# Kernel tuning notes

Measured on AMD Instinct MI355X. Metric: run time of the kernel, lower is better.

## Reference

```python
import jax, jax.numpy as jnp
import numpy as np
import math

B, S, D_MODEL, H, CLIP = 4, 1024, 1024, 16, 16
HEAD_DIM = D_MODEL // H
NEG = -1e6


def setup_inputs() -> dict:
    key = jax.random.key(0)
    ks = jax.random.split(key, 10)
    scale = 1.0 / math.sqrt(D_MODEL)
    return {
        "queries": jax.random.normal(ks[0], (B, S, D_MODEL), jnp.float32),
        "keys": jax.random.normal(ks[1], (B, S, D_MODEL), jnp.float32),
        "values": jax.random.normal(ks[2], (B, S, D_MODEL), jnp.float32),
        "valid_lens": jax.random.randint(ks[3], (B,), 1, S + 1),
        "Wq": jax.random.normal(ks[4], (D_MODEL, D_MODEL), jnp.float32) * scale,
        "Wk": jax.random.normal(ks[5], (D_MODEL, D_MODEL), jnp.float32) * scale,
        "Wv": jax.random.normal(ks[6], (D_MODEL, D_MODEL), jnp.float32) * scale,
        "Wo": jax.random.normal(ks[7], (D_MODEL, D_MODEL), jnp.float32) * scale,
        "Ek": jax.random.normal(ks[8], (2 * CLIP + 1, HEAD_DIM), jnp.float32),
        "Ev": jax.random.normal(ks[9], (2 * CLIP + 1, HEAD_DIM), jnp.float32),
    }


def _split_heads(x):
    # [B, S, D] -> [B*H, S, head_dim]
    b, s, _ = x.shape
    return x.reshape(b, s, H, HEAD_DIM).transpose(0, 2, 1, 3).reshape(b * H, s, HEAD_DIM)


def reference(queries, keys, values, valid_lens, Wq, Wk, Wv, Wo, Ek, Ev):
    q = _split_heads(queries @ Wq.T)  # [BH, S, d]
    k = _split_heads(keys @ Wk.T)
    v = _split_heads(values @ Wv.T)

    # relative-position tables, shared across batch and heads: [Sq, Sk, d]
    rng = jnp.arange(S)
    dist = jnp.clip(rng[None, :] - rng[:, None], -CLIP, CLIP) + CLIP
    pos_k = Ek[dist]
    pos_v = Ev[dist]

    scores = jnp.einsum('bqd,bkd->bqk', q, k) + jnp.einsum('bqd,qkd->bqk', q, pos_k)
    scores = scores / math.sqrt(HEAD_DIM)

    vl = jnp.repeat(valid_lens, H)  # [B*H]
    mask = jnp.arange(S)[None, None, :] < vl[:, None, None]
    attn = jax.nn.softmax(jnp.where(mask, scores, NEG), axis=-1)

    out = jnp.einsum('bqk,bkd->bqd', attn, v) + jnp.einsum('bqk,qkd->bqd', attn, pos_v)

    # merge heads: [B*H, S, d] -> [B, S, D]
    out = out.reshape(B, H, S, HEAD_DIM).transpose(0, 2, 1, 3).reshape(B, S, D_MODEL)
    return out @ Wo.T
```

## Files before the change

### kernel.cpp

```cpp
#include <hip/hip_runtime.h>


typedef __attribute__((ext_vector_type(8))) short short8;
typedef __attribute__((ext_vector_type(4))) float floatx4;

__device__ __forceinline__ unsigned short f2bf(float f) {
  union { float f; unsigned u; } v; v.f = f;
  return (unsigned short)((v.u + 0x7fffu + ((v.u >> 16) & 1u)) >> 16);
}
__device__ __forceinline__ unsigned packbf(float lo, float hi) {
  return ((unsigned)f2bf(hi) << 16) | (unsigned)f2bf(lo);
}

__device__ __forceinline__ void gld16(const void* g, void* l) {
  __builtin_amdgcn_global_load_lds(
      (const __attribute__((address_space(1))) unsigned*)g,
      (__attribute__((address_space(3))) unsigned*)l, 16, 0, 0);
}

#define WS_XQ  ((size_t)0)
#define WS_XK  ((size_t)4194304)
#define WS_XV  ((size_t)8388608)
#define WS_W   ((size_t)12582912)
#define WS_EKB ((size_t)16777216)
#define WS_EVT ((size_t)16781312)
#define WS_QB  ((size_t)16785408)
#define WS_KB  ((size_t)20979712)
#define WS_VT  ((size_t)25174016)
#define WS_OB  ((size_t)0)

__global__ __launch_bounds__(256) void convert_all_kernel(
    const float* __restrict__ q, const float* __restrict__ k,
    const float* __restrict__ v,
    const float* __restrict__ wq, const float* __restrict__ wk,
    const float* __restrict__ wv, const float* __restrict__ wo,
    const float* __restrict__ Ek, const float* __restrict__ Ev,
    const int* __restrict__ valid_lens, unsigned short* __restrict__ ws) {
  int z = blockIdx.z;
  if (z < 3) {
    const float* src = z == 0 ? q : (z == 1 ? k : v);
    unsigned short* dst = ws + (size_t)z * 4194304;
    size_t i = ((size_t)blockIdx.x * 256 + threadIdx.x) * 8;
    if (z > 0) {
      int b = (int)(i >> 20), s = (int)((i >> 10) & 1023);
      if (s >= valid_lens[b]) return;
    }
    float4 a = *(const float4*)(src + i);
    float4 bb = *(const float4*)(src + i + 4);
    uint4 o = { packbf(a.x, a.y), packbf(a.z, a.w), packbf(bb.x, bb.y), packbf(bb.z, bb.w) };
    *(uint4*)(dst + i) = o;
  } else if (z < 7) {
    if (blockIdx.x >= 512) return;
    const float* src = (z == 3) ? wq : (z == 4 ? wk : (z == 5 ? wv : wo));
    unsigned short* dst = ws + WS_W + (size_t)(z - 3) * 1048576;
    size_t i = ((size_t)blockIdx.x * 256 + threadIdx.x) * 8;
    float4 a = *(const float4*)(src + i);
    float4 bb = *(const float4*)(src + i + 4);
    uint4 o = { packbf(a.x, a.y), packbf(a.z, a.w), packbf(bb.x, bb.y), packbf(bb.z, bb.w) };
    *(uint4*)(dst + i) = o;
  } else {
    if (blockIdx.x >= 4) return;
    int gid = blockIdx.x * 256 + threadIdx.x;
    unsigned short* ekb = ws + WS_EKB;
    int i0 = gid * 8;
    unsigned short vals[8];
#pragma unroll
    for (int u = 0; u < 8; u++) {
      int i = i0 + u;
      if (i < 4096) {
        int t = i >> 6, d = i & 63;
        vals[u] = (t < 33) ? f2bf(Ek[t * 64 + d]) : (unsigned short)0;
      } else {
        int j = i - 4096;
        int d = j >> 6, t = j & 63;
        vals[u] = (t < 33) ? f2bf(Ev[t * 64 + d]) : (unsigned short)0;
      }
    }
    *(uint4*)(ekb + i0) = *(uint4*)vals;
  }
}

__device__ __forceinline__ void gemm128_body(
    const unsigned short* __restrict__ A, const unsigned short* __restrict__ W,
    unsigned short* __restrict__ Cb, float* __restrict__ Cf, int mode, float scale) {
  __shared__ unsigned short sA[128 * 32];
  __shared__ unsigned short sB[128 * 32];
  const int tid = threadIdx.x, wave = tid >> 6, lane = tid & 63;
  const int lr = lane & 15, lq = lane >> 4;
  const int wr = wave >> 1, wc = wave & 1;
  const int m0 = blockIdx.y * 128, n0 = blockIdx.x * 128;
  const int srow = lane >> 2, scol = (lane & 3) * 8;

  const unsigned short* gA0 = A + (size_t)(m0 + wave * 16 + srow) * 1024 + scol;
  const unsigned short* gA1 = gA0 + (size_t)64 * 1024;
  const unsigned short* gB0 = W + (size_t)(n0 + wave * 16 + srow) * 1024 + scol;
  const unsigned short* gB1 = gB0 + (size_t)64 * 1024;
  unsigned short* lA0 = sA + wave * 512;  unsigned short* lA1 = lA0 + 2048;
  unsigned short* lB0 = sB + wave * 512;  unsigned short* lB1 = lB0 + 2048;

  floatx4 acc[4][4];
#pragma unroll
  for (int mi = 0; mi < 4; mi++)
#pragma unroll
    for (int ni = 0; ni < 4; ni++) acc[mi][ni] = (floatx4){0.f, 0.f, 0.f, 0.f};

  for (int k0 = 0; k0 < 1024; k0 += 32) {
    gld16(gA0 + k0, lA0); gld16(gA1 + k0, lA1);
    gld16(gB0 + k0, lB0); gld16(gB1 + k0, lB1);
    __syncthreads();
    short8 af[4], bf[4];
#pragma unroll
    for (int mi = 0; mi < 4; mi++)
      af[mi] = *(const short8*)(sA + (wr * 64 + mi * 16 + lr) * 32 + lq * 8);
#pragma unroll
    for (int ni = 0; ni < 4; ni++)
      bf[ni] = *(const short8*)(sB + (wc * 64 + ni * 16 + lr) * 32 + lq * 8);
#pragma unroll
    for (int mi = 0; mi < 4; mi++)
#pragma unroll
      for (int ni = 0; ni < 4; ni++)
        acc[mi][ni] = __builtin_amdgcn_mfma_f32_16x16x32_bf16(af[mi], bf[ni], acc[mi][ni], 0, 0, 0);
    __syncthreads();
  }

  if (mode == 2) {
#pragma unroll
    for (int mi = 0; mi < 4; mi++)
#pragma unroll
      for (int ni = 0; ni < 4; ni++) {
        int col = n0 + wc * 64 + ni * 16 + lr;
        int h = col >> 6, d = col & 63;
        int rowg = m0 + wr * 64 + mi * 16 + lq * 4;
        int b = rowg >> 10, s = rowg & 1023;
        int bh = b * 16 + h;
        uint2 pk;
        pk.x = packbf(acc[mi][ni][0], acc[mi][ni][1]);
        pk.y = packbf(acc[mi][ni][2], acc[mi][ni][3]);
        size_t off = (size_t)bh * 65536
                   + (size_t)((s >> 6) * 8 + (d >> 4) * 2 + ((s >> 5) & 1)) * 512
                   + (size_t)((((s >> 3) & 3) * 16) + (d & 15)) * 8 + (s & 7);
        *(uint2*)(Cb + off) = pk;
      }
  } else if (mode == 1) {
#pragma unroll
    for (int mi = 0; mi < 4; mi++)
#pragma unroll
      for (int ni = 0; ni < 4; ni++)
#pragma unroll
        for (int r = 0; r < 4; r++) {
          int rowg = m0 + wr * 64 + mi * 16 + lq * 4 + r;
          int col = n0 + wc * 64 + ni * 16 + lr;
          int b = rowg >> 10, s = rowg & 1023;
          int h = col >> 6, d = col & 63;
          int bh = b * 16 + h;
          size_t off = (size_t)bh * 65536
                     + (size_t)((s >> 6) * 8 + ((s & 63) >> 4) * 2 + (d >> 5)) * 512
                     + (size_t)((((d & 31) >> 3) * 16) + (s & 15)) * 8 + (d & 7);
          Cb[off] = f2bf(acc[mi][ni][r]);
        }
  } else if (mode == 3) {
#pragma unroll
    for (int mi = 0; mi < 4; mi++)
#pragma unroll
      for (int ni = 0; ni < 4; ni++)
#pragma unroll
        for (int r = 0; r < 4; r++) {
          int row = m0 + wr * 64 + mi * 16 + lq * 4 + r;
          int col = n0 + wc * 64 + ni * 16 + lr;
          Cf[(size_t)row * 1024 + col] = acc[mi][ni][r];
        }
  } else {
#pragma unroll
    for (int mi = 0; mi < 4; mi++)
#pragma unroll
      for (int ni = 0; ni < 4; ni++)
#pragma unroll
        for (int r = 0; r < 4; r++) {
          int row = m0 + wr * 64 + mi * 16 + lq * 4 + r;
          int col = n0 + wc * 64 + ni * 16 + lr;
          Cb[(size_t)row * 1024 + col] = f2bf(acc[mi][ni][r] * scale);
        }
  }
}

__global__ __launch_bounds__(256, 3) void proj_qkv_kernel(
    unsigned short* __restrict__ ws, const int* __restrict__ valid_lens) {
  int z = blockIdx.z;
  if (z > 0) {
    int m0 = blockIdx.y * 128;
    if ((m0 & 1023) >= valid_lens[m0 >> 10]) return;
  }
  const unsigned short* A = ws + (size_t)z * 4194304;
  const unsigned short* W = ws + WS_W + (size_t)z * 1048576;
  unsigned short* Cb = (z == 0) ? ws + WS_QB : (z == 1 ? ws + WS_KB : ws + WS_VT);
  int mode = (z == 2) ? 2 : (z == 0 ? 0 : 1);
  float scale = (z == 0) ? 0.125f : 1.0f;
  gemm128_body(A, W, Cb, nullptr, mode, scale);
}

__global__ __launch_bounds__(256, 3) void out_proj_kernel(
    const unsigned short* __restrict__ Ob, const unsigned short* __restrict__ Wo,
    float* __restrict__ out) {
  gemm128_body(Ob, Wo, nullptr, out, 3, 1.f);
}

__global__ __launch_bounds__(64, 2) void attn_rpr_kernel(
    const unsigned short* __restrict__ Qb, const unsigned short* __restrict__ Kf,
    const unsigned short* __restrict__ Vf, const int* __restrict__ valid_lens,
    const unsigned short* __restrict__ Ekb, const unsigned short* __restrict__ Evtb,
    unsigned short* __restrict__ Ob) {
  __shared__ unsigned short sP[32 * 72];
  __shared__ float sQE[32 * 34];
  __shared__ float sW[32 * 34];

  const int lane = threadIdx.x;
  const int lr = lane & 15, lq = lane >> 4;
  const int bh = blockIdx.x, qx = blockIdx.y;
  const int b = bh >> 4;
  const int vlen = valid_lens[b];
  const int i0 = qx * 32;
  const int colh = (bh & 15) * 64;
  const size_t bat = (size_t)b * 1024 * 1024;
  const int rbase = lq * 4;

  for (int i = lane; i < 32 * 34; i += 64) sW[i] = 0.f;

  const unsigned short* gQ = Qb + bat + (size_t)(i0 + lr) * 1024 + colh + lq * 8;
  short8 aq0[2], aq1[2];
#pragma unroll
  for (int g = 0; g < 2; g++) {
    aq0[g] = *(const short8*)(gQ + (size_t)g * 16 * 1024);
    aq1[g] = *(const short8*)(gQ + (size_t)g * 16 * 1024 + 32);
  }

#pragma unroll
  for (int ni = 0; ni < 3; ni++) {
    short8 be0 = *(const short8*)(Ekb + (ni * 16 + lr) * 64 + lq * 8);
    short8 be1 = *(const short8*)(Ekb + (ni * 16 + lr) * 64 + 32 + lq * 8);
    int t = ni * 16 + lr;
#pragma unroll
    for (int g = 0; g < 2; g++) {
      floatx4 aqe = (floatx4){0.f, 0.f, 0.f, 0.f};
      aqe = __builtin_amdgcn_mfma_f32_16x16x32_bf16(aq0[g], be0, aqe, 0, 0, 0);
      aqe = __builtin_amdgcn_mfma_f32_16x16x32_bf16(aq1[g], be1, aqe, 0, 0, 0);
      if (t < 33)
#pragma unroll
        for (int r = 0; r < 4; r++) sQE[(g * 16 + rbase + r) * 34 + t] = aqe[r];
    }
  }

  floatx4 acc_o[2][4];
#pragma unroll
  for (int g = 0; g < 2; g++)
#pragma unroll
    for (int nd = 0; nd < 4; nd++) acc_o[g][nd] = (floatx4){0.f, 0.f, 0.f, 0.f};
  float rs0[2][4] = {{0.f,0.f,0.f,0.f},{0.f,0.f,0.f,0.f}};
  float rs32[2][4] = {{0.f,0.f,0.f,0.f},{0.f,0.f,0.f,0.f}};

  const int vcl = vlen < 1024 ? vlen : 1024;
  const int kt_max = (vcl + 63) >> 6;

  const unsigned short* gKf = Kf + (size_t)bh * 65536 + lane * 8;
  const unsigned short* gVf = Vf + (size_t)bh * 65536 + lane * 8;

  for (int kt = 0; kt < kt_max; kt++) {
    const int j0 = kt * 64;

    short8 bk[4][2], bv[4][2];
#pragma unroll
    for (int ni = 0; ni < 4; ni++) {
      bk[ni][0] = *(const short8*)(gKf + (size_t)(kt * 8 + ni * 2 + 0) * 512);
      bk[ni][1] = *(const short8*)(gKf + (size_t)(kt * 8 + ni * 2 + 1) * 512);
    }
#pragma unroll
    for (int nd = 0; nd < 4; nd++) {
      bv[nd][0] = *(const short8*)(gVf + (size_t)(kt * 8 + nd * 2 + 0) * 512);
      bv[nd][1] = *(const short8*)(gVf + (size_t)(kt * 8 + nd * 2 + 1) * 512);
    }

    floatx4 accs[2][4];
    __builtin_amdgcn_s_setprio(1);
#pragma unroll
    for (int g = 0; g < 2; g++)
#pragma unroll
      for (int ni = 0; ni < 4; ni++) {
        accs[g][ni] = (floatx4){0.f, 0.f, 0.f, 0.f};
        accs[g][ni] = __builtin_amdgcn_mfma_f32_16x16x32_bf16(aq0[g], bk[ni][0], accs[g][ni], 0, 0, 0);
        accs[g][ni] = __builtin_amdgcn_mfma_f32_16x16x32_bf16(aq1[g], bk[ni][1], accs[g][ni], 0, 0, 0);
      }
    __builtin_amdgcn_s_setprio(0);

    const bool general = (j0 > i0 - 79) && (j0 < i0 + 47);
    if (!general) {
      const bool hi = (j0 >= i0 + 47);
      const int tconst = hi ? 32 : 0;
#pragma unroll
      for (int g = 0; g < 2; g++) {
        float qe[4];
#pragma unroll
        for (int r = 0; r < 4; r++) qe[r] = sQE[(g * 16 + rbase + r) * 34 + tconst];
#pragma unroll
        for (int ni = 0; ni < 4; ni++)
#pragma unroll
          for (int r = 0; r < 4; r++) {
            int j_g = j0 + ni * 16 + lr;
            float pv = (j_g < vlen) ? __expf(accs[g][ni][r] + qe[r]) : 0.f;
            if (hi) rs32[g][r] += pv; else rs0[g][r] += pv;
            sP[(g * 16 + rbase + r) * 72 + ni * 16 + lr] = f2bf(pv);
          }
      }
    } else {
#pragma unroll
      for (int g = 0; g < 2; g++)
#pragma unroll
        for (int ni = 0; ni < 4; ni++)
#pragma unroll
          for (int r = 0; r < 4; r++) {
            int i_g = i0 + g * 16 + rbase + r;
            int j_g = j0 + ni * 16 + lr;
            int dd = j_g - i_g; dd = dd < -16 ? -16 : (dd > 16 ? 16 : dd);
            int t = dd + 16;
            float pv = (j_g < vlen) ? __expf(accs[g][ni][r] + sQE[(g * 16 + rbase + r) * 34 + t]) : 0.f;
            atomicAdd(&sW[(g * 16 + rbase + r) * 34 + t], pv);
            sP[(g * 16 + rbase + r) * 72 + ni * 16 + lr] = f2bf(pv);
          }
    }

    __builtin_amdgcn_s_setprio(1);
#pragma unroll
    for (int g = 0; g < 2; g++) {
      short8 ap0 = *(const short8*)(sP + (g * 16 + lr) * 72 + lq * 8);
      short8 ap1 = *(const short8*)(sP + (g * 16 + lr) * 72 + 32 + lq * 8);
#pragma unroll
      for (int nd = 0; nd < 4; nd++) {
        acc_o[g][nd] = __builtin_amdgcn_mfma_f32_16x16x32_bf16(ap0, bv[nd][0], acc_o[g][nd], 0, 0, 0);
        acc_o[g][nd] = __builtin_amdgcn_mfma_f32_16x16x32_bf16(ap1, bv[nd][1], acc_o[g][nd], 0, 0, 0);
      }
    }
    __builtin_amdgcn_s_setprio(0);
  }

#pragma unroll
  for (int x = 1; x < 16; x <<= 1)
#pragma unroll
    for (int g = 0; g < 2; g++)
#pragma unroll
      for (int r = 0; r < 4; r++) {
        rs0[g][r] += __shfl_xor(rs0[g][r], x, 64);
        rs32[g][r] += __shfl_xor(rs32[g][r], x, 64);
      }
  if (lr == 0)
#pragma unroll
    for (int g = 0; g < 2; g++)
#pragma unroll
      for (int r = 0; r < 4; r++) {
        sW[(g * 16 + rbase + r) * 34 + 0] += rs0[g][r];
        sW[(g * 16 + rbase + r) * 34 + 32] += rs32[g][r];
      }

  {
    int row = lane >> 2;
    int c0 = (lane & 3) * 16;
    unsigned* sP32 = (unsigned*)sP;
#pragma unroll
    for (int g = 0; g < 2; g++)
#pragma unroll
      for (int q = 0; q < 8; q++) {
        int t0 = c0 + 2 * q, t1 = t0 + 1;
        float w0 = (t0 < 33) ? sW[(g * 16 + row) * 34 + t0] : 0.f;
        float w1 = (t1 < 33) ? sW[(g * 16 + row) * 34 + t1] : 0.f;
        sP32[(g * 16 + row) * 36 + (c0 >> 1) + q] = packbf(w0, w1);
      }
  }
#pragma unroll
  for (int g = 0; g < 2; g++) {
    short8 aw0 = *(const short8*)(sP + (g * 16 + lr) * 72 + lq * 8);
    short8 aw1 = *(const short8*)(sP + (g * 16 + lr) * 72 + 32 + lq * 8);
#pragma unroll
    for (int nd = 0; nd < 4; nd++) {
      short8 be0 = *(const short8*)(Evtb + (nd * 16 + lr) * 64 + lq * 8);
      short8 be1 = *(const short8*)(Evtb + (nd * 16 + lr) * 64 + 32 + lq * 8);
      acc_o[g][nd] = __builtin_amdgcn_mfma_f32_16x16x32_bf16(aw0, be0, acc_o[g][nd], 0, 0, 0);
      acc_o[g][nd] = __builtin_amdgcn_mfma_f32_16x16x32_bf16(aw1, be1, acc_o[g][nd], 0, 0, 0);
    }
  }

#pragma unroll
  for (int g = 0; g < 2; g++) {
    float linv[4];
#pragma unroll
    for (int r = 0; r < 4; r++) {
      float l = 0.f;
#pragma unroll
      for (int t = 0; t < 33; t++) l += sW[(g * 16 + rbase + r) * 34 + t];
      linv[r] = 1.f / l;
    }
#pragma unroll
    for (int nd = 0; nd < 4; nd++)
#pragma unroll
      for (int r = 0; r < 4; r++) {
        int row = i0 + g * 16 + rbase + r;
        Ob[bat + (size_t)row * 1024 + colh + nd * 16 + lr] =
            f2bf(acc_o[g][nd][r] * linv[r]);
      }
  }
}

extern "C" void kernel_launch(void* const* d_in, const int* in_sizes, int n_in,
                              void* d_out, int out_size, void* d_ws, size_t ws_size,
                              hipStream_t stream) {
  const float* queries = (const float*)d_in[0];
  const float* keys    = (const float*)d_in[1];
  const float* values  = (const float*)d_in[2];
  const int* valid_lens = (const int*)d_in[3];
  const float* Wq = (const float*)d_in[4];
  const float* Wk = (const float*)d_in[5];
  const float* Wv = (const float*)d_in[6];
  const float* Wo = (const float*)d_in[7];
  const float* Ek = (const float*)d_in[8];
  const float* Ev = (const float*)d_in[9];
  float* out = (float*)d_out;
  unsigned short* ws = (unsigned short*)d_ws;

  convert_all_kernel<<<dim3(2048, 1, 8), 256, 0, stream>>>(
      queries, keys, values, Wq, Wk, Wv, Wo, Ek, Ev, valid_lens, ws);
  proj_qkv_kernel<<<dim3(8, 32, 3), 256, 0, stream>>>(ws, valid_lens);
  attn_rpr_kernel<<<dim3(64, 32), 64, 0, stream>>>(
      ws + WS_QB, ws + WS_KB, ws + WS_VT, valid_lens, ws + WS_EKB, ws + WS_EVT, ws + WS_OB);
  out_proj_kernel<<<dim3(8, 32), 256, 0, stream>>>(ws + WS_OB, ws + WS_W + 3145728, out);
}
```

Baseline: 222.5 us.

## Use dedicated 64x128 out-proj GEMM and remap attention grid block order

Swaps the generic 128x128 GEMM body in the output projection for a dedicated 64x128-tile kernel with simple global-to-LDS loads and occupancy 4, doubling the block count to 512 to fill more CUs. The attention launch is flattened to a 1D grid, with an index remap so consecutive blocks cover all 16 heads of a batch for a given query tile, and batches are interleaved. The remap is meant to spread work across batches with different valid lengths and improve L2 locality. The new GEMM drops whatever pipelining gemm128_body had, since it syncs twice per 32-wide K step without double buffering.

Measured after the change: 212.6 us (median of 2 runs). 4.4% less time.

```diff
diff --git a/kernel.cpp b/kernel.cpp
--- a/kernel.cpp
+++ b/kernel.cpp
@@ -198,10 +198,58 @@
   gemm128_body(A, W, Cb, nullptr, mode, scale);
 }
 
-__global__ __launch_bounds__(256, 3) void out_proj_kernel(
+__global__ __launch_bounds__(256, 4) void out_proj_kernel(
     const unsigned short* __restrict__ Ob, const unsigned short* __restrict__ Wo,
     float* __restrict__ out) {
-  gemm128_body(Ob, Wo, nullptr, out, 3, 1.f);
+  __shared__ unsigned short sA[64 * 32];
+  __shared__ unsigned short sB[128 * 32];
+  const int tid = threadIdx.x, wave = tid >> 6, lane = tid & 63;
+  const int lr = lane & 15, lq = lane >> 4;
+  const int wr = wave >> 1, wc = wave & 1;
+  const int m0 = blockIdx.y * 64, n0 = blockIdx.x * 128;
+  const int srow = lane >> 2, scol = (lane & 3) * 8;
+
+  const unsigned short* gA0 = Ob + (size_t)(m0 + wave * 16 + srow) * 1024 + scol;
+  const unsigned short* gB0 = Wo + (size_t)(n0 + wave * 16 + srow) * 1024 + scol;
+  const unsigned short* gB1 = gB0 + (size_t)64 * 1024;
+  unsigned short* lA0 = sA + wave * 512;
+  unsigned short* lB0 = sB + wave * 512;  unsigned short* lB1 = lB0 + 2048;
+
+  floatx4 acc[2][4];
+#pragma unroll
+  for (int mi = 0; mi < 2; mi++)
+#pragma unroll
+    for (int ni = 0; ni < 4; ni++) acc[mi][ni] = (floatx4){0.f, 0.f, 0.f, 0.f};
+
+  for (int k0 = 0; k0 < 1024; k0 += 32) {
+    gld16(gA0 + k0, lA0);
+    gld16(gB0 + k0, lB0); gld16(gB1 + k0, lB1);
+    __syncthreads();
+    short8 af[2], bf[4];
+#pragma unroll
+    for (int mi = 0; mi < 2; mi++)
+      af[mi] = *(const short8*)(sA + (wr * 32 + mi * 16 + lr) * 32 + lq * 8);
+#pragma unroll
+    for (int ni = 0; ni < 4; ni++)
+      bf[ni] = *(const short8*)(sB + (wc * 64 + ni * 16 + lr) * 32 + lq * 8);
+#pragma unroll
+    for (int mi = 0; mi < 2; mi++)
+#pragma unroll
+      for (int ni = 0; ni < 4; ni++)
+        acc[mi][ni] = __builtin_amdgcn_mfma_f32_16x16x32_bf16(af[mi], bf[ni], acc[mi][ni], 0, 0, 0);
+    __syncthreads();
+  }
+
+#pragma unroll
+  for (int mi = 0; mi < 2; mi++)
+#pragma unroll
+    for (int ni = 0; ni < 4; ni++)
+#pragma unroll
+      for (int r = 0; r < 4; r++) {
+        int row = m0 + wr * 32 + mi * 16 + lq * 4 + r;
+        int col = n0 + wc * 64 + ni * 16 + lr;
+        out[(size_t)row * 1024 + col] = acc[mi][ni][r];
+      }
 }
 
 __global__ __launch_bounds__(64, 2) void attn_rpr_kernel(
@@ -215,8 +263,11 @@
 
   const int lane = threadIdx.x;
   const int lr = lane & 15, lq = lane >> 4;
-  const int bh = blockIdx.x, qx = blockIdx.y;
-  const int b = bh >> 4;
+  const int x = blockIdx.x;
+  const int rr = x >> 8, ss = x & 255;
+  const int b = rr & 3;
+  const int bh = b * 16 + (ss & 15);
+  const int qx = ((rr >> 2) << 4) + (ss >> 4);
   const int vlen = valid_lens[b];
   const int i0 = qx * 32;
   const int colh = (bh & 15) * 64;
@@ -341,13 +392,13 @@
   }
 
 #pragma unroll
-  for (int x = 1; x < 16; x <<= 1)
+  for (int x2 = 1; x2 < 16; x2 <<= 1)
 #pragma unroll
     for (int g = 0; g < 2; g++)
 #pragma unroll
       for (int r = 0; r < 4; r++) {
-        rs0[g][r] += __shfl_xor(rs0[g][r], x, 64);
-        rs32[g][r] += __shfl_xor(rs32[g][r], x, 64);
+        rs0[g][r] += __shfl_xor(rs0[g][r], x2, 64);
+        rs32[g][r] += __shfl_xor(rs32[g][r], x2, 64);
       }
   if (lr == 0)
 #pragma unroll
@@ -425,7 +476,7 @@
   convert_all_kernel<<<dim3(2048, 1, 8), 256, 0, stream>>>(
       queries, keys, values, Wq, Wk, Wv, Wo, Ek, Ev, valid_lens, ws);
   proj_qkv_kernel<<<dim3(8, 32, 3), 256, 0, stream>>>(ws, valid_lens);
-  attn_rpr_kernel<<<dim3(64, 32), 64, 0, stream>>>(
+  attn_rpr_kernel<<<dim3(2048), 64, 0, stream>>>(
       ws + WS_QB, ws + WS_KB, ws + WS_VT, valid_lens, ws + WS_EKB, ws + WS_EVT, ws + WS_OB);
-  out_proj_kernel<<<dim3(8, 32), 256, 0, stream>>>(ws + WS_OB, ws + WS_W + 3145728, out);
-}
+  out_proj_kernel<<<dim3(8, 64), 256, 0, stream>>>(ws + WS_OB, ws + WS_W + 3145728, out);
+}
```
